# Kernel tuning notes

Measured on AMD Instinct MI355X. Metric: run time of the kernel, lower is better.

The kernel has to match this reference:

```python
import jax, jax.numpy as jnp
import numpy as np

V, F, H, R = 10000, 768, 768, 49
B, T = 128, 32


def setup_inputs() -> dict:
    key = jax.random.key(0)
    ks = jax.random.split(key, 12)
    s = lambda *sh: 1.0 / np.sqrt(sh[-1])
    return {
        "features": jax.random.normal(ks[0], (B, R, F), jnp.float32),
        "captions": jax.random.randint(ks[1], (B, T), 0, V),
        "emb_W": jax.random.normal(ks[2], (V, H), jnp.float32),
        "attn_W": jax.random.normal(ks[3], (H, F + H), jnp.float32) * s(H, F + H),
        "attn_b": jnp.zeros((H,), jnp.float32),
        "attnv_W": jax.random.normal(ks[4], (1, H), jnp.float32) * s(1, H),
        "attnv_b": jnp.zeros((1,), jnp.float32),
        "W_ih": jax.random.normal(ks[5], (4 * H, H + F), jnp.float32) * s(1, H),
        "W_hh": jax.random.normal(ks[6], (4 * H, H), jnp.float32) * s(1, H),
        "b_ih": jnp.zeros((4 * H,), jnp.float32),
        "b_hh": jnp.zeros((4 * H,), jnp.float32),
        "fc_W": jax.random.normal(ks[7], (V, H), jnp.float32) * s(V, H),
        "fc_b": jnp.zeros((V,), jnp.float32),
    }


def reference(features, captions, emb_W, attn_W, attn_b, attnv_W, attnv_b,
              W_ih, W_hh, b_ih, b_hh, fc_W, fc_b):
    # initial hidden state (hidden_state=None branch)
    h0 = jnp.tanh(features.mean(axis=1))           # [B,H]
    c0 = jnp.zeros_like(h0)                        # [B,H]
    emb = emb_W[captions]                          # [B,T,H]

    # split attn_linear weight into feature/hidden parts; feature projection is
    # time-invariant so compute once outside the scan.
    Wf, Wh = attn_W[:, :F], attn_W[:, F:]
    feat_proj = jnp.einsum('brf,hf->brh', features, Wf)   # [B,R,H]
    v = attnv_W[0]                                 # [H]
    bias = b_ih + b_hh                             # [4H]

    def step(carry, emb_t):
        h, c = carry
        attn_hidden = jnp.tanh(feat_proj + (h @ Wh.T)[:, None, :] + attn_b)  # [B,R,H]
        scores = attn_hidden @ v + attnv_b[0]      # [B,R]
        alpha = jax.nn.softmax(scores, axis=1)
        context = jnp.einsum('br,brf->bf', alpha, features)  # [B,F]
        x = jnp.concatenate([emb_t, context], axis=1)        # [B,H+F]
        gates = x @ W_ih.T + h @ W_hh.T + bias     # [B,4H]
        i, f, g, o = jnp.split(gates, 4, axis=1)
        c_new = jax.nn.sigmoid(f) * c + jax.nn.sigmoid(i) * jnp.tanh(g)
        h_new = jax.nn.sigmoid(o) * jnp.tanh(c_new)
        out_t = h_new @ fc_W.T + fc_b              # [B,V] (dropout = identity, eval)
        return (h_new, c_new), out_t

    (h, c), outs = jax.lax.scan(step, (h0, c0), jnp.swapaxes(emb, 0, 1))
    outputs = jnp.swapaxes(outs, 0, 1)             # [B,T,V]
    return outputs, (h, c)
```

## Files before the change

### kernel.cpp

```cpp
#include <hip/hip_runtime.h>


typedef _Float16 f16x8 __attribute__((ext_vector_type(8)));
typedef _Float16 f16x4 __attribute__((ext_vector_type(4)));
typedef float f32x4 __attribute__((ext_vector_type(4)));

#define NB 128
#define NT 32
#define NV 10000
#define NH 768
#define NR 49
#define OUT_ELEMS 40960000

__device__ __forceinline__ float fast_tanh(float x) {
  x = fminf(9.f, fmaxf(-9.f, x));
  float e = __expf(2.f * x);
  return (e - 1.f) / (e + 1.f);
}
__device__ __forceinline__ float sigm(float x) { return 1.f / (1.f + __expf(-x)); }

__device__ __forceinline__ void gld16(const void* g, void* l) {
  __builtin_amdgcn_global_load_lds((const __attribute__((address_space(1))) void*)g,
                                   (__attribute__((address_space(3))) void*)l, 16, 0, 0);
}

template <int BM, int BN, int EPI>
__global__ __launch_bounds__(256) void gemm_f16(
    const _Float16* __restrict__ A, int lda,
    const _Float16* __restrict__ Bt, int ldb,
    void* __restrict__ Cv, const float* __restrict__ bias,
    int M, int N, int ksteps, int ksplit) {
  constexpr int BK = 64;
  __shared__ __attribute__((aligned(16))) _Float16 sA[BM * BK];
  __shared__ __attribute__((aligned(16))) _Float16 sB[BN * BK];
  const int tid = threadIdx.x;
  const int m0 = blockIdx.x * BM, n0 = blockIdx.y * BN;
  const int z = blockIdx.z;
  A += (size_t)z * ksplit;
  Bt += (size_t)z * ksplit;

  constexpr int WM = BM / 2, WN = BN / 2;
  constexpr int MF = WM / 16, NF = WN / 16;
  const int wid = tid >> 6, lane = tid & 63;
  const int wr = wid >> 1, wc = wid & 1;
  const int lr = lane & 15;
  const int lk = (lane >> 4) * 8;

  f32x4 acc[MF][NF] = {};

  for (int kt = 0; kt < ksteps; ++kt) {
    const int kbase = kt * BK;
#pragma unroll
    for (int i = 0; i < BM / 32; i++) {
      int idx = tid + i * 256;
      int row = idx >> 3, seg = idx & 7;
      gld16(A + (size_t)(m0 + row) * lda + kbase + seg * 8, sA + idx * 8);
    }
#pragma unroll
    for (int i = 0; i < BN / 32; i++) {
      int idx = tid + i * 256;
      int row = idx >> 3, seg = idx & 7;
      int gr = n0 + row;
      if (gr >= N) gr = N - 1;
      gld16(Bt + (size_t)gr * ldb + kbase + seg * 8, sB + idx * 8);
    }
    __syncthreads();
#pragma unroll
    for (int kk = 0; kk < 2; ++kk) {
      f16x8 af[MF], bf[NF];
#pragma unroll
      for (int m = 0; m < MF; m++)
        af[m] = *(const f16x8*)&sA[(wr * WM + m * 16 + lr) * BK + kk * 32 + lk];
#pragma unroll
      for (int n = 0; n < NF; n++)
        bf[n] = *(const f16x8*)&sB[(wc * WN + n * 16 + lr) * BK + kk * 32 + lk];
#pragma unroll
      for (int m = 0; m < MF; m++)
#pragma unroll
        for (int n = 0; n < NF; n++)
          acc[m][n] = __builtin_amdgcn_mfma_f32_16x16x32_f16(af[m], bf[n], acc[m][n], 0, 0, 0);
    }
    __syncthreads();
  }

  const int rowb = (lane >> 4) * 4;
#pragma unroll
  for (int m = 0; m < MF; m++) {
    int gm = m0 + wr * WM + m * 16 + rowb;
#pragma unroll
    for (int n = 0; n < NF; n++) {
      int gn = n0 + wc * WN + n * 16 + lr;
#pragma unroll
      for (int j = 0; j < 4; j++) {
        int r = gm + j;
        if (EPI == 1) {
          float* C = (float*)Cv + (size_t)z * M * N;
          C[(size_t)r * N + gn] = acc[m][n][j];
        } else if (EPI == 2) {
          if (gn < N) {
            int t = r >> 7, b = r & 127;
            ((float*)Cv)[((size_t)(b * NT + t)) * NV + gn] = acc[m][n][j] + bias[gn];
          }
        } else if (EPI == 3) {
          ((_Float16*)Cv)[(size_t)r * N + gn] = (_Float16)(acc[m][n][j] + bias[gn]);
        } else {
          ((_Float16*)Cv)[(size_t)r * N + gn] = (_Float16)acc[m][n][j];
        }
      }
    }
  }
}

__global__ void k_f32_to_f16(const float* __restrict__ src, _Float16* __restrict__ dst, int n) {
  int i = blockIdx.x * 256 + threadIdx.x;
  if (i < n) dst[i] = (_Float16)src[i];
}

__global__ void k_wih_split(const float* __restrict__ W_ih, _Float16* __restrict__ We,
                            _Float16* __restrict__ Wc) {
  int j = blockIdx.x;
  int k = blockIdx.y * 256 + threadIdx.x;
  We[(size_t)j * NH + k] = (_Float16)W_ih[(size_t)j * 1536 + k];
  Wc[(size_t)j * NH + k] = (_Float16)W_ih[(size_t)j * 1536 + 768 + k];
}

__global__ void k_w1cat(const float* __restrict__ attn_W, const float* __restrict__ W_hh,
                        _Float16* __restrict__ W1) {
  int j = blockIdx.x;
  int k = blockIdx.y * 256 + threadIdx.x;
  float v = (j < NH) ? attn_W[(size_t)j * 1536 + 768 + k]
                     : W_hh[(size_t)(j - NH) * NH + k];
  W1[(size_t)j * NH + k] = (_Float16)v;
}

__global__ void k_emb2(const int* __restrict__ captions, const float* __restrict__ emb_W,
                       _Float16* __restrict__ emb16) {
  int row = blockIdx.x;
  int k = blockIdx.y * 256 + threadIdx.x;
  int t = row >> 7, b = row & 127;
  int tok = captions[b * NT + t];
  emb16[(size_t)row * NH + k] = (_Float16)emb_W[(size_t)tok * NH + k];
}

__global__ void k_init(const float* __restrict__ features, float* __restrict__ h,
                       float* __restrict__ c, _Float16* __restrict__ h16) {
  int b = blockIdx.x;
  int f = blockIdx.y * 256 + threadIdx.x;
  float s = 0.f;
#pragma unroll 7
  for (int r = 0; r < NR; r++) s += features[((size_t)(b * NR + r)) * NH + f];
  float h0 = tanhf(s * (1.f / 49.f));
  h[b * NH + f] = h0;
  c[b * NH + f] = 0.f;
  h16[(size_t)b * NH + f] = (_Float16)h0;
}

__global__ __launch_bounds__(256) void k_scores(
    const _Float16* __restrict__ fp, const float* __restrict__ g1,
    const float* __restrict__ v, float* __restrict__ sc) {
  int wid = threadIdx.x >> 6, lane = threadIdx.x & 63;
  int p = blockIdx.x * 4 + wid;
  int b = p / NR;
  const _Float16* fpr = fp + (size_t)p * NH;
  const float* hw0 = g1 + (size_t)b * 3840;
  const float* hw1 = g1 + (size_t)NB * 3840 + (size_t)b * 3840;
  float s = 0.f;
#pragma unroll
  for (int it = 0; it < 3; it++) {
    int h = it * 256 + lane * 4;
    f16x4 fv = *(const f16x4*)(fpr + h);
    f32x4 a0 = *(const f32x4*)(hw0 + h);
    f32x4 a1 = *(const f32x4*)(hw1 + h);
    f32x4 vv = *(const f32x4*)(v + h);
#pragma unroll
    for (int j = 0; j < 4; j++) s += fast_tanh((float)fv[j] + a0[j] + a1[j]) * vv[j];
  }
#pragma unroll
  for (int off = 32; off; off >>= 1) s += __shfl_down(s, off);
  if (lane == 0) sc[p] = s;
}

__global__ __launch_bounds__(256) void k_ctx(const float* __restrict__ sc,
                                             const _Float16* __restrict__ feat16,
                                             _Float16* __restrict__ ctx16) {
  __shared__ float al[64];
  int b = blockIdx.x, tid = threadIdx.x;
  if (tid < 64) {
    float s = (tid < NR) ? sc[b * NR + tid] : -1e30f;
    float m = s;
#pragma unroll
    for (int off = 32; off; off >>= 1) m = fmaxf(m, __shfl_xor(m, off));
    float e = (tid < NR) ? __expf(s - m) : 0.f;
    float su = e;
#pragma unroll
    for (int off = 32; off; off >>= 1) su += __shfl_xor(su, off);
    al[tid] = e / su;
  }
  __syncthreads();
  int f = blockIdx.y * 256 + tid;
  const _Float16* fb = feat16 + (size_t)b * NR * NH + f;
  float acc = 0.f;
#pragma unroll
  for (int r = 0; r < NR; r++) acc += al[r] * (float)fb[(size_t)r * NH];
  ctx16[(size_t)b * NH + f] = (_Float16)acc;
}

__global__ void k_lstm2(const _Float16* __restrict__ ge_t, const float* __restrict__ g1,
                        const float* __restrict__ g2, const float* __restrict__ b_ih,
                        const float* __restrict__ b_hh, float* __restrict__ h,
                        float* __restrict__ c, _Float16* __restrict__ h16,
                        _Float16* __restrict__ Hall_t) {
  int b = blockIdx.x;
  int hh = blockIdx.y * 256 + threadIdx.x;
  const _Float16* ge = ge_t + (size_t)b * 3072;
  const float* a0 = g1 + (size_t)b * 3840 + 768;
  const float* a1 = g1 + (size_t)NB * 3840 + (size_t)b * 3840 + 768;
  const float* c0 = g2 + (size_t)b * 3072;
  const float* c1 = g2 + (size_t)NB * 3072 + (size_t)b * 3072;
  float gi = (float)ge[hh] + a0[hh] + a1[hh] + c0[hh] + c1[hh] + b_ih[hh] + b_hh[hh];
  float gf = (float)ge[768 + hh] + a0[768 + hh] + a1[768 + hh] + c0[768 + hh] + c1[768 + hh] +
             b_ih[768 + hh] + b_hh[768 + hh];
  float gg = (float)ge[1536 + hh] + a0[1536 + hh] + a1[1536 + hh] + c0[1536 + hh] +
             c1[1536 + hh] + b_ih[1536 + hh] + b_hh[1536 + hh];
  float go = (float)ge[2304 + hh] + a0[2304 + hh] + a1[2304 + hh] + c0[2304 + hh] +
             c1[2304 + hh] + b_ih[2304 + hh] + b_hh[2304 + hh];
  float i_ = sigm(gi), f_ = sigm(gf), g_ = fast_tanh(gg), o_ = sigm(go);
  float cn = f_ * c[b * NH + hh] + i_ * g_;
  float hn = o_ * fast_tanh(cn);
  c[b * NH + hh] = cn;
  h[b * NH + hh] = hn;
  h16[(size_t)b * NH + hh] = (_Float16)hn;
  Hall_t[(size_t)b * NH + hh] = (_Float16)hn;
}

__global__ void k_tail(const float* __restrict__ h, const float* __restrict__ c,
                       float* __restrict__ out) {
  int i = blockIdx.x * 256 + threadIdx.x;
  out[OUT_ELEMS + i] = h[i];
  out[OUT_ELEMS + NB * NH + i] = c[i];
}

extern "C" void kernel_launch(void* const* d_in, const int* in_sizes, int n_in,
                              void* d_out, int out_size, void* d_ws, size_t ws_size,
                              hipStream_t stream) {
  const float* features = (const float*)d_in[0];
  const int* captions = (const int*)d_in[1];
  const float* emb_W = (const float*)d_in[2];
  const float* attn_W = (const float*)d_in[3];
  const float* attn_b = (const float*)d_in[4];
  const float* attnv_W = (const float*)d_in[5];
  const float* W_ih = (const float*)d_in[7];
  const float* W_hh = (const float*)d_in[8];
  const float* b_ih = (const float*)d_in[9];
  const float* b_hh = (const float*)d_in[10];
  const float* fc_W = (const float*)d_in[11];
  const float* fc_b = (const float*)d_in[12];
  float* out = (float*)d_out;

  char* p = (char*)d_ws;
  _Float16* Gemb16 = (_Float16*)p;  p += 25165824;
  _Float16* fcW16 = Gemb16;
  _Float16* emb16 = (_Float16*)p;   p += 6291456;
  _Float16* feat16 = (_Float16*)p;  p += 9633792;
  _Float16* fp16 = (_Float16*)p;    p += 9633792;
  _Float16* attnW16 = (_Float16*)p; p += 2359296;
  _Float16* W1 = (_Float16*)p;      p += 5898240;
  _Float16* We16 = (_Float16*)p;    p += 4718592;
  _Float16* Wc16 = (_Float16*)p;    p += 4718592;
  _Float16* H_all = (_Float16*)p;   p += 6291456;
  float* g1 = (float*)p;            p += 3932160;
  float* g2 = (float*)p;            p += 3145728;
  float* scores = (float*)p;        p += 25088;
  _Float16* ctx16 = (_Float16*)p;   p += 196608;
  _Float16* h16 = (_Float16*)p;     p += 196608;
  float* hbuf = (float*)p;          p += 393216;
  float* cbuf = (float*)p;          p += 393216;

  k_f32_to_f16<<<dim3(18816), 256, 0, stream>>>(features, feat16, 4816896);
  k_f32_to_f16<<<dim3(4608), 256, 0, stream>>>(attn_W, attnW16, 1179648);
  k_wih_split<<<dim3(3072, 3), 256, 0, stream>>>(W_ih, We16, Wc16);
  k_w1cat<<<dim3(3840, 3), 256, 0, stream>>>(attn_W, W_hh, W1);
  k_emb2<<<dim3(4096, 3), 256, 0, stream>>>(captions, emb_W, emb16);
  k_init<<<dim3(128, 3), 256, 0, stream>>>(features, hbuf, cbuf, h16);
  gemm_f16<128, 128, 3><<<dim3(49, 6, 1), 256, 0, stream>>>(
      feat16, 768, attnW16, 1536, fp16, attn_b, 6272, 768, 12, 0);
  gemm_f16<128, 128, 4><<<dim3(32, 24, 1), 256, 0, stream>>>(
      emb16, 768, We16, 768, Gemb16, nullptr, 4096, 3072, 12, 0);

  for (int t = 0; t < NT; t++) {
    if (t > 0)
      k_lstm2<<<dim3(128, 3), 256, 0, stream>>>(
          Gemb16 + (size_t)(t - 1) * NB * 3072, g1, g2, b_ih, b_hh, hbuf, cbuf, h16,
          H_all + (size_t)(t - 1) * NB * NH);
    gemm_f16<64, 64, 1><<<dim3(2, 60, 2), 256, 0, stream>>>(
        h16, 768, W1, 768, g1, nullptr, 128, 3840, 6, 384);
    k_scores<<<dim3(1568), 256, 0, stream>>>(fp16, g1, attnv_W, scores);
    k_ctx<<<dim3(128, 3), 256, 0, stream>>>(scores, feat16, ctx16);
    gemm_f16<64, 64, 1><<<dim3(2, 48, 2), 256, 0, stream>>>(
        ctx16, 768, Wc16, 768, g2, nullptr, 128, 3072, 6, 384);
  }
  k_lstm2<<<dim3(128, 3), 256, 0, stream>>>(
      Gemb16 + (size_t)(NT - 1) * NB * 3072, g1, g2, b_ih, b_hh, hbuf, cbuf, h16,
      H_all + (size_t)(NT - 1) * NB * NH);

  k_f32_to_f16<<<dim3(30000), 256, 0, stream>>>(fc_W, fcW16, 7680000);
  gemm_f16<128, 128, 2><<<dim3(32, 79, 1), 256, 0, stream>>>(
      H_all, 768, fcW16, 768, out, fc_b, 4096, 10000, 12, 0);
  k_tail<<<dim3(384), 256, 0, stream>>>(hbuf, cbuf, out);
}
```

Measured before the change: 1.132 ms.

## Fuse attention scores+context and context GEMM+LSTM cell, interleave gate weights

```diff
diff --git a/kernel.cpp b/kernel.cpp
--- a/kernel.cpp
+++ b/kernel.cpp
@@ -111,26 +111,167 @@
   }
 }
 
+__global__ __launch_bounds__(256) void k_g2lstm(
+    const _Float16* __restrict__ A, const _Float16* __restrict__ Bt,
+    const float* __restrict__ g1, const _Float16* __restrict__ ge_t,
+    const float* __restrict__ bias_int, float* __restrict__ c, float* __restrict__ h,
+    _Float16* __restrict__ h16, _Float16* __restrict__ Hall_t) {
+  constexpr int BK = 64;
+  __shared__ __attribute__((aligned(16))) _Float16 sA[64 * BK];
+  __shared__ __attribute__((aligned(16))) _Float16 sB[64 * BK];
+  __shared__ float sC[64 * 68];
+  const int tid = threadIdx.x;
+  const int m0 = blockIdx.x * 64, n0 = blockIdx.y * 64;
+
+  const int wid = tid >> 6, lane = tid & 63;
+  const int wr = wid >> 1, wc = wid & 1;
+  const int lr = lane & 15;
+  const int lk = (lane >> 4) * 8;
+
+  f32x4 acc[2][2] = {};
+
+  for (int kt = 0; kt < 12; ++kt) {
+    const int kbase = kt * BK;
+#pragma unroll
+    for (int i = 0; i < 2; i++) {
+      int idx = tid + i * 256;
+      int row = idx >> 3, seg = idx & 7;
+      gld16(A + (size_t)(m0 + row) * NH + kbase + seg * 8, sA + idx * 8);
+      gld16(Bt + (size_t)(n0 + row) * NH + kbase + seg * 8, sB + idx * 8);
+    }
+    __syncthreads();
+#pragma unroll
+    for (int kk = 0; kk < 2; ++kk) {
+      f16x8 af[2], bf[2];
+#pragma unroll
+      for (int m = 0; m < 2; m++)
+        af[m] = *(const f16x8*)&sA[(wr * 32 + m * 16 + lr) * BK + kk * 32 + lk];
+#pragma unroll
+      for (int n = 0; n < 2; n++)
+        bf[n] = *(const f16x8*)&sB[(wc * 32 + n * 16 + lr) * BK + kk * 32 + lk];
+#pragma unroll
+      for (int m = 0; m < 2; m++)
+#pragma unroll
+        for (int n = 0; n < 2; n++)
+          acc[m][n] = __builtin_amdgcn_mfma_f32_16x16x32_f16(af[m], bf[n], acc[m][n], 0, 0, 0);
+    }
+    __syncthreads();
+  }
+
+  const int rowb = (lane >> 4) * 4;
+#pragma unroll
+  for (int m = 0; m < 2; m++) {
+    int bl = wr * 32 + m * 16 + rowb;
+#pragma unroll
+    for (int n = 0; n < 2; n++) {
+      int jl = wc * 32 + n * 16 + lr;
+#pragma unroll
+      for (int j = 0; j < 4; j++) sC[(bl + j) * 68 + jl] = acc[m][n][j];
+    }
+  }
+  __syncthreads();
+
+  const int b_l = tid & 63;
+  const int b_g = m0 + b_l;
+#pragma unroll
+  for (int i = 0; i < 4; i++) {
+    int hh_l = (tid >> 6) * 4 + i;
+    int hh_g = (n0 >> 2) + hh_l;
+    f32x4 g = *(const f32x4*)&sC[b_l * 68 + 4 * hh_l];
+    f32x4 p0 = *(const f32x4*)&g1[(size_t)b_g * 3840 + 768 + 4 * hh_g];
+    f32x4 p1 = *(const f32x4*)&g1[(size_t)NB * 3840 + (size_t)b_g * 3840 + 768 + 4 * hh_g];
+    f16x4 ge = *(const f16x4*)&ge_t[(size_t)b_g * 3072 + 4 * hh_g];
+    f32x4 bi = *(const f32x4*)&bias_int[4 * hh_g];
+    float gi = g[0] + p0[0] + p1[0] + (float)ge[0] + bi[0];
+    float gf = g[1] + p0[1] + p1[1] + (float)ge[1] + bi[1];
+    float gg = g[2] + p0[2] + p1[2] + (float)ge[2] + bi[2];
+    float go = g[3] + p0[3] + p1[3] + (float)ge[3] + bi[3];
+    float cn = sigm(gf) * c[b_g * NH + hh_g] + sigm(gi) * fast_tanh(gg);
+    float hn = sigm(go) * fast_tanh(cn);
+    c[b_g * NH + hh_g] = cn;
+    h[b_g * NH + hh_g] = hn;
+    h16[(size_t)b_g * NH + hh_g] = (_Float16)hn;
+    Hall_t[(size_t)b_g * NH + hh_g] = (_Float16)hn;
+  }
+}
+
+__global__ __launch_bounds__(256) void k_attn(
+    const _Float16* __restrict__ fp, const float* __restrict__ g1,
+    const float* __restrict__ v, const _Float16* __restrict__ feat16,
+    _Float16* __restrict__ ctx16) {
+  __shared__ float hw[NH], vv[NH], sc[NR], al[64];
+  const int b = blockIdx.x, tid = threadIdx.x;
+  for (int i = tid; i < NH; i += 256) {
+    hw[i] = g1[(size_t)b * 3840 + i] + g1[(size_t)NB * 3840 + (size_t)b * 3840 + i];
+    vv[i] = v[i];
+  }
+  __syncthreads();
+  const int wid = tid >> 6, lane = tid & 63;
+  for (int r = wid; r < NR; r += 4) {
+    const _Float16* fpr = fp + (size_t)(b * NR + r) * NH;
+    float s = 0.f;
+#pragma unroll
+    for (int it = 0; it < 3; it++) {
+      int hh = it * 256 + lane * 4;
+      f16x4 fv = *(const f16x4*)(fpr + hh);
+#pragma unroll
+      for (int j = 0; j < 4; j++) s += fast_tanh((float)fv[j] + hw[hh + j]) * vv[hh + j];
+    }
+#pragma unroll
+    for (int off = 32; off; off >>= 1) s += __shfl_down(s, off);
+    if (lane == 0) sc[r] = s;
+  }
+  __syncthreads();
+  if (tid < 64) {
+    float s = (tid < NR) ? sc[tid] : -1e30f;
+    float m = s;
+#pragma unroll
+    for (int off = 32; off; off >>= 1) m = fmaxf(m, __shfl_xor(m, off));
+    float e = (tid < NR) ? __expf(s - m) : 0.f;
+    float su = e;
+#pragma unroll
+    for (int off = 32; off; off >>= 1) su += __shfl_xor(su, off);
+    al[tid] = e / su;
+  }
+  __syncthreads();
+#pragma unroll
+  for (int j = 0; j < 3; j++) {
+    int f = tid + j * 256;
+    const _Float16* fb = feat16 + (size_t)b * NR * NH + f;
+    float acc = 0.f;
+#pragma unroll
+    for (int r = 0; r < NR; r++) acc += al[r] * (float)fb[(size_t)r * NH];
+    ctx16[(size_t)b * NH + f] = (_Float16)acc;
+  }
+}
+
 __global__ void k_f32_to_f16(const float* __restrict__ src, _Float16* __restrict__ dst, int n) {
   int i = blockIdx.x * 256 + threadIdx.x;
   if (i < n) dst[i] = (_Float16)src[i];
 }
 
-__global__ void k_wih_split(const float* __restrict__ W_ih, _Float16* __restrict__ We,
-                            _Float16* __restrict__ Wc) {
+__global__ void k_wint(const float* __restrict__ W_ih, const float* __restrict__ W_hh,
+                       _Float16* __restrict__ We_int, _Float16* __restrict__ Wc_int,
+                       _Float16* __restrict__ W1) {
+  int jp = blockIdx.x;
+  int k = blockIdx.y * 256 + threadIdx.x;
+  int src = (jp & 3) * NH + (jp >> 2);
+  We_int[(size_t)jp * NH + k] = (_Float16)W_ih[(size_t)src * 1536 + k];
+  Wc_int[(size_t)jp * NH + k] = (_Float16)W_ih[(size_t)src * 1536 + 768 + k];
+  W1[(size_t)(768 + jp) * NH + k] = (_Float16)W_hh[(size_t)src * NH + k];
+}
+
+__global__ void k_wh(const float* __restrict__ attn_W, _Float16* __restrict__ W1) {
   int j = blockIdx.x;
   int k = blockIdx.y * 256 + threadIdx.x;
-  We[(size_t)j * NH + k] = (_Float16)W_ih[(size_t)j * 1536 + k];
-  Wc[(size_t)j * NH + k] = (_Float16)W_ih[(size_t)j * 1536 + 768 + k];
-}
-
-__global__ void k_w1cat(const float* __restrict__ attn_W, const float* __restrict__ W_hh,
-                        _Float16* __restrict__ W1) {
-  int j = blockIdx.x;
-  int k = blockIdx.y * 256 + threadIdx.x;
-  float v = (j < NH) ? attn_W[(size_t)j * 1536 + 768 + k]
-                     : W_hh[(size_t)(j - NH) * NH + k];
-  W1[(size_t)j * NH + k] = (_Float16)v;
+  W1[(size_t)j * NH + k] = (_Float16)attn_W[(size_t)j * 1536 + 768 + k];
+}
+
+__global__ void k_bias(const float* __restrict__ b_ih, const float* __restrict__ b_hh,
+                       float* __restrict__ bias_int) {
+  int jp = blockIdx.x * 256 + threadIdx.x;
+  int src = (jp & 3) * NH + (jp >> 2);
+  bias_int[jp] = b_ih[src] + b_hh[src];
 }
 
 __global__ void k_emb2(const int* __restrict__ captions, const float* __restrict__ emb_W,
@@ -153,84 +294,6 @@
   h[b * NH + f] = h0;
   c[b * NH + f] = 0.f;
   h16[(size_t)b * NH + f] = (_Float16)h0;
-}
-
-__global__ __launch_bounds__(256) void k_scores(
-    const _Float16* __restrict__ fp, const float* __restrict__ g1,
-    const float* __restrict__ v, float* __restrict__ sc) {
-  int wid = threadIdx.x >> 6, lane = threadIdx.x & 63;
-  int p = blockIdx.x * 4 + wid;
-  int b = p / NR;
-  const _Float16* fpr = fp + (size_t)p * NH;
-  const float* hw0 = g1 + (size_t)b * 3840;
-  const float* hw1 = g1 + (size_t)NB * 3840 + (size_t)b * 3840;
-  float s = 0.f;
-#pragma unroll
-  for (int it = 0; it < 3; it++) {
-    int h = it * 256 + lane * 4;
-    f16x4 fv = *(const f16x4*)(fpr + h);
-    f32x4 a0 = *(const f32x4*)(hw0 + h);
-    f32x4 a1 = *(const f32x4*)(hw1 + h);
-    f32x4 vv = *(const f32x4*)(v + h);
-#pragma unroll
-    for (int j = 0; j < 4; j++) s += fast_tanh((float)fv[j] + a0[j] + a1[j]) * vv[j];
-  }
-#pragma unroll
-  for (int off = 32; off; off >>= 1) s += __shfl_down(s, off);
-  if (lane == 0) sc[p] = s;
-}
-
-__global__ __launch_bounds__(256) void k_ctx(const float* __restrict__ sc,
-                                             const _Float16* __restrict__ feat16,
-                                             _Float16* __restrict__ ctx16) {
-  __shared__ float al[64];
-  int b = blockIdx.x, tid = threadIdx.x;
-  if (tid < 64) {
-    float s = (tid < NR) ? sc[b * NR + tid] : -1e30f;
-    float m = s;
-#pragma unroll
-    for (int off = 32; off; off >>= 1) m = fmaxf(m, __shfl_xor(m, off));
-    float e = (tid < NR) ? __expf(s - m) : 0.f;
-    float su = e;
-#pragma unroll
-    for (int off = 32; off; off >>= 1) su += __shfl_xor(su, off);
-    al[tid] = e / su;
-  }
-  __syncthreads();
-  int f = blockIdx.y * 256 + tid;
-  const _Float16* fb = feat16 + (size_t)b * NR * NH + f;
-  float acc = 0.f;
-#pragma unroll
-  for (int r = 0; r < NR; r++) acc += al[r] * (float)fb[(size_t)r * NH];
-  ctx16[(size_t)b * NH + f] = (_Float16)acc;
-}
-
-__global__ void k_lstm2(const _Float16* __restrict__ ge_t, const float* __restrict__ g1,
-                        const float* __restrict__ g2, const float* __restrict__ b_ih,
-                        const float* __restrict__ b_hh, float* __restrict__ h,
-                        float* __restrict__ c, _Float16* __restrict__ h16,
-                        _Float16* __restrict__ Hall_t) {
-  int b = blockIdx.x;
-  int hh = blockIdx.y * 256 + threadIdx.x;
-  const _Float16* ge = ge_t + (size_t)b * 3072;
-  const float* a0 = g1 + (size_t)b * 3840 + 768;
-  const float* a1 = g1 + (size_t)NB * 3840 + (size_t)b * 3840 + 768;
-  const float* c0 = g2 + (size_t)b * 3072;
-  const float* c1 = g2 + (size_t)NB * 3072 + (size_t)b * 3072;
-  float gi = (float)ge[hh] + a0[hh] + a1[hh] + c0[hh] + c1[hh] + b_ih[hh] + b_hh[hh];
-  float gf = (float)ge[768 + hh] + a0[768 + hh] + a1[768 + hh] + c0[768 + hh] + c1[768 + hh] +
-             b_ih[768 + hh] + b_hh[768 + hh];
-  float gg = (float)ge[1536 + hh] + a0[1536 + hh] + a1[1536 + hh] + c0[1536 + hh] +
-             c1[1536 + hh] + b_ih[1536 + hh] + b_hh[1536 + hh];
-  float go = (float)ge[2304 + hh] + a0[2304 + hh] + a1[2304 + hh] + c0[2304 + hh] +
-             c1[2304 + hh] + b_ih[2304 + hh] + b_hh[2304 + hh];
-  float i_ = sigm(gi), f_ = sigm(gf), g_ = fast_tanh(gg), o_ = sigm(go);
-  float cn = f_ * c[b * NH + hh] + i_ * g_;
-  float hn = o_ * fast_tanh(cn);
-  c[b * NH + hh] = cn;
-  h[b * NH + hh] = hn;
-  h16[(size_t)b * NH + hh] = (_Float16)hn;
-  Hall_t[(size_t)b * NH + hh] = (_Float16)hn;
 }
 
 __global__ void k_tail(const float* __restrict__ h, const float* __restrict__ c,
@@ -265,12 +328,11 @@
   _Float16* fp16 = (_Float16*)p;    p += 9633792;
   _Float16* attnW16 = (_Float16*)p; p += 2359296;
   _Float16* W1 = (_Float16*)p;      p += 5898240;
-  _Float16* We16 = (_Float16*)p;    p += 4718592;
-  _Float16* Wc16 = (_Float16*)p;    p += 4718592;
+  _Float16* We_int = (_Float16*)p;  p += 4718592;
+  _Float16* Wc_int = (_Float16*)p;  p += 4718592;
   _Float16* H_all = (_Float16*)p;   p += 6291456;
   float* g1 = (float*)p;            p += 3932160;
-  float* g2 = (float*)p;            p += 3145728;
-  float* scores = (float*)p;        p += 25088;
+  float* bias_int = (float*)p;      p += 12288;
   _Float16* ctx16 = (_Float16*)p;   p += 196608;
   _Float16* h16 = (_Float16*)p;     p += 196608;
   float* hbuf = (float*)p;          p += 393216;
@@ -278,30 +340,24 @@
 
   k_f32_to_f16<<<dim3(18816), 256, 0, stream>>>(features, feat16, 4816896);
   k_f32_to_f16<<<dim3(4608), 256, 0, stream>>>(attn_W, attnW16, 1179648);
-  k_wih_split<<<dim3(3072, 3), 256, 0, stream>>>(W_ih, We16, Wc16);
-  k_w1cat<<<dim3(3840, 3), 256, 0, stream>>>(attn_W, W_hh, W1);
+  k_wint<<<dim3(3072, 3), 256, 0, stream>>>(W_ih, W_hh, We_int, Wc_int, W1);
+  k_wh<<<dim3(768, 3), 256, 0, stream>>>(attn_W, W1);
+  k_bias<<<dim3(12), 256, 0, stream>>>(b_ih, b_hh, bias_int);
   k_emb2<<<dim3(4096, 3), 256, 0, stream>>>(captions, emb_W, emb16);
   k_init<<<dim3(128, 3), 256, 0, stream>>>(features, hbuf, cbuf, h16);
   gemm_f16<128, 128, 3><<<dim3(49, 6, 1), 256, 0, stream>>>(
       feat16, 768, attnW16, 1536, fp16, attn_b, 6272, 768, 12, 0);
   gemm_f16<128, 128, 4><<<dim3(32, 24, 1), 256, 0, stream>>>(
-      emb16, 768, We16, 768, Gemb16, nullptr, 4096, 3072, 12, 0);
+      emb16, 768, We_int, 768, Gemb16, nullptr, 4096, 3072, 12, 0);
 
   for (int t = 0; t < NT; t++) {
-    if (t > 0)
-      k_lstm2<<<dim3(128, 3), 256, 0, stream>>>(
-          Gemb16 + (size_t)(t - 1) * NB * 3072, g1, g2, b_ih, b_hh, hbuf, cbuf, h16,
-          H_all + (size_t)(t - 1) * NB * NH);
     gemm_f16<64, 64, 1><<<dim3(2, 60, 2), 256, 0, stream>>>(
         h16, 768, W1, 768, g1, nullptr, 128, 3840, 6, 384);
-    k_scores<<<dim3(1568), 256, 0, stream>>>(fp16, g1, attnv_W, scores);
-    k_ctx<<<dim3(128, 3), 256, 0, stream>>>(scores, feat16, ctx16);
-    gemm_f16<64, 64, 1><<<dim3(2, 48, 2), 256, 0, stream>>>(
-        ctx16, 768, Wc16, 768, g2, nullptr, 128, 3072, 6, 384);
-  }
-  k_lstm2<<<dim3(128, 3), 256, 0, stream>>>(
-      Gemb16 + (size_t)(NT - 1) * NB * 3072, g1, g2, b_ih, b_hh, hbuf, cbuf, h16,
-      H_all + (size_t)(NT - 1) * NB * NH);
+    k_attn<<<dim3(128), 256, 0, stream>>>(fp16, g1, attnv_W, feat16, ctx16);
+    k_g2lstm<<<dim3(2, 48), 256, 0, stream>>>(
+        ctx16, Wc_int, g1, Gemb16 + (size_t)t * NB * 3072, bias_int, cbuf, hbuf, h16,
+        H_all + (size_t)t * NB * NH);
+  }
 
   k_f32_to_f16<<<dim3(30000), 256, 0, stream>>>(fc_W, fcW16, 7680000);
   gemm_f16<128, 128, 2><<<dim3(32, 79, 1), 256, 0, stream>>>(
```

Result: slower. 1.572 ms (+38.9%).
